# Kernel tuning notes

Measured on AMD Instinct MI355X. Metric: run time of the kernel, lower is better.

The kernel has to match this reference:

```python
import jax, jax.numpy as jnp
import numpy as np

N, E, F_IN, C, H12, H3, NCLS = 10000, 160000, 50, 256, 4, 6, 121


def gat_conv(x, src, dst, W, a_src, a_dst, b, heads, out_ch, concat, n):
    # x: [n, f_in]; W: [f_in, heads*out_ch]; a_*: [heads, out_ch]; src/dst: [e]
    h = (x @ W).reshape(n, heads, out_ch)
    # per-edge attention logits, LeakyReLU(0.2) as in PyG GATConv
    alpha = jax.nn.leaky_relu((h * a_src).sum(-1)[src] + (h * a_dst).sum(-1)[dst], 0.2)  # [e, heads]
    # segment softmax over incoming edges of each destination node
    amax = jax.ops.segment_max(alpha, dst, num_segments=n)
    ex = jnp.exp(alpha - amax[dst])
    denom = jax.ops.segment_sum(ex, dst, num_segments=n)
    w = ex / (denom[dst] + 1e-16)
    out = jax.ops.segment_sum(h[src] * w[..., None], dst, num_segments=n)  # [n, heads, out_ch]
    out = out.reshape(n, heads * out_ch) if concat else out.mean(axis=1)
    return out + b


def setup_inputs() -> dict:
    key = jax.random.key(0)
    ks = jax.random.split(key, 22)
    s = 0.05
    nrm = lambda k, shp: jax.random.normal(k, shp, jnp.float32) * s
    D = C * H12  # 1024
    return {
        "x": jax.random.normal(ks[0], (N, F_IN), jnp.float32),
        "edge_index": jax.random.randint(ks[1], (2, E), 0, N, dtype=jnp.int32),
        "W1": nrm(ks[2], (F_IN, H12 * C)), "a_src1": nrm(ks[3], (H12, C)), "a_dst1": nrm(ks[4], (H12, C)), "b1": jnp.zeros((H12 * C,), jnp.float32),
        "lW1": nrm(ks[5], (F_IN, D)), "lb1": jnp.zeros((D,), jnp.float32),
        "W2": nrm(ks[6], (D, H12 * C)), "a_src2": nrm(ks[7], (H12, C)), "a_dst2": nrm(ks[8], (H12, C)), "b2": jnp.zeros((H12 * C,), jnp.float32),
        "lW2": nrm(ks[9], (D, D)), "lb2": jnp.zeros((D,), jnp.float32),
        "W3": nrm(ks[10], (D, H3 * NCLS)), "a_src3": nrm(ks[11], (H3, NCLS)), "a_dst3": nrm(ks[12], (H3, NCLS)), "b3": jnp.zeros((NCLS,), jnp.float32),
        "lW3": nrm(ks[13], (D, NCLS)), "lb3": jnp.zeros((NCLS,), jnp.float32),
    }


def reference(x, edge_index, W1, a_src1, a_dst1, b1, lW1, lb1,
              W2, a_src2, a_dst2, b2, lW2, lb2,
              W3, a_src3, a_dst3, b3, lW3, lb3):
    n = x.shape[0]
    loop = jnp.arange(n, dtype=edge_index.dtype)  # self loops (PyG default)
    src = jnp.concatenate([edge_index[0], loop])
    dst = jnp.concatenate([edge_index[1], loop])
    h = jax.nn.elu(gat_conv(x, src, dst, W1, a_src1, a_dst1, b1, H12, C, True, n) + x @ lW1 + lb1)
    h = jax.nn.elu(gat_conv(h, src, dst, W2, a_src2, a_dst2, b2, H12, C, True, n) + h @ lW2 + lb2)
    return gat_conv(h, src, dst, W3, a_src3, a_dst3, b3, H3, NCLS, False, n) + h @ lW3 + lb3
```

## Files before the change

### kernel.cpp

```cpp
#include <hip/hip_runtime.h>
#include <cstdint>
#include <cstddef>

#define NN 10000
#define EE 160000
#define EN_ (EE + NN)
#define MPAD 10112
#define MT 79
#define CAP 512

typedef short s16x8 __attribute__((ext_vector_type(8)));
typedef float f32x4 __attribute__((ext_vector_type(4)));
typedef unsigned short u16;

__device__ __forceinline__ u16 f2bf(float f) {
  uint32_t u = __float_as_uint(f);
  uint32_t r = (u + 0x7fffu + ((u >> 16) & 1u)) >> 16;
  return (u16)r;
}
__device__ __forceinline__ float b2f(u16 u) {
  return __uint_as_float(((uint32_t)u) << 16);
}
__device__ __forceinline__ float b2f_lo(uint32_t p) { return __uint_as_float(p << 16); }
__device__ __forceinline__ float b2f_hi(uint32_t p) { return __uint_as_float(p & 0xffff0000u); }
__device__ __forceinline__ float lrelu02(float x) { return x > 0.f ? x : 0.2f * x; }
__device__ __forceinline__ float eluf(float x) { return x > 0.f ? x : (__expf(x) - 1.f); }

__global__ void k_count(const int* __restrict__ ei, int* __restrict__ cnt) {
  int e = blockIdx.x * blockDim.x + threadIdx.x;
  if (e >= EN_) return;
  int d = (e < EE) ? ei[EE + e] : (e - EE);
  atomicAdd(&cnt[d], 1);
}

__global__ __launch_bounds__(1024) void k_scan(const int* __restrict__ cnt, int* __restrict__ off) {
  __shared__ int sums[1024];
  int t = threadIdx.x;
  const int per = (NN + 1023) / 1024;
  int base = t * per;
  int local = 0;
  for (int j = 0; j < per; ++j) {
    int idx = base + j;
    if (idx < NN) local += cnt[idx];
  }
  sums[t] = local;
  __syncthreads();
  for (int s = 1; s < 1024; s <<= 1) {
    int v = (t >= s) ? sums[t - s] : 0;
    __syncthreads();
    sums[t] += v;
    __syncthreads();
  }
  int run = (t == 0) ? 0 : sums[t - 1];
  for (int j = 0; j < per; ++j) {
    int idx = base + j;
    if (idx < NN) { off[idx] = run; run += cnt[idx]; }
  }
  if (t == 1023) off[NN] = EN_;
}

__global__ void k_fill(const int* __restrict__ ei, const int* __restrict__ off,
                       int* __restrict__ cursor, int* __restrict__ csr_src) {
  int e = blockIdx.x * blockDim.x + threadIdx.x;
  if (e >= EN_) return;
  int s, d;
  if (e < EE) { s = ei[e]; d = ei[EE + e]; } else { s = d = e - EE; }
  int p = atomicAdd(&cursor[d], 1);
  csr_src[off[d] + p] = s;
}

#define PREP_BLOCKS 3490
__global__ __launch_bounds__(256) void k_prep(
    const float* __restrict__ x, u16* __restrict__ xb,
    const float* __restrict__ W1, const float* __restrict__ lW1,
    const float* __restrict__ W2, const float* __restrict__ lW2,
    const float* __restrict__ W3, const float* __restrict__ lW3,
    u16* __restrict__ wtc1, u16* __restrict__ wtc2, u16* __restrict__ wtc3,
    const float* __restrict__ lb1, const float* __restrict__ lb2,
    const float* __restrict__ lb3, float* __restrict__ fb,
    u16* __restrict__ bufX, int* __restrict__ cnt) {
  int b = blockIdx.x, t = threadIdx.x;
  if (b < 768) {
    const float* W; u16* Bt; int K, N, Kpad, nb, kb;
    if (b < 16)       { W = W1;  Bt = wtc1;                       K = 50;   N = 1024; Kpad = 64;   nb = b;      kb = 0; }
    else if (b < 32)  { W = lW1; Bt = wtc1 + (size_t)1024 * 64;   K = 50;   N = 1024; Kpad = 64;   nb = b - 16; kb = 0; }
    else if (b < 288) { int r = b - 32;  W = W2;  Bt = wtc2;                         K = 1024; N = 1024; Kpad = 1024; nb = r & 15; kb = r >> 4; }
    else if (b < 544) { int r = b - 288; W = lW2; Bt = wtc2 + (size_t)1024 * 1024;   K = 1024; N = 1024; Kpad = 1024; nb = r & 15; kb = r >> 4; }
    else if (b < 736) { int r = b - 544; W = W3;  Bt = wtc3;                         K = 1024; N = 726;  Kpad = 1024; nb = r % 12; kb = r / 12; }
    else              { int r = b - 736; W = lW3; Bt = wtc3 + (size_t)768 * 1024;    K = 1024; N = 121;  Kpad = 1024; nb = r & 1;  kb = r >> 1; }
    __shared__ float tile[64][65];
    int kbase = kb * 64, nbase = nb * 64;
    int nl = t & 63, kl0 = t >> 6;
#pragma unroll
    for (int j = 0; j < 16; ++j) {
      int k = kbase + kl0 + j * 4, n = nbase + nl;
      tile[kl0 + j * 4][nl] = (k < K && n < N) ? W[(size_t)k * N + n] : 0.f;
    }
    __syncthreads();
    int nr = t >> 2, kc = (t & 3) * 16;
    uint32_t pk[8];
#pragma unroll
    for (int j = 0; j < 8; ++j) {
      pk[j] = (uint32_t)f2bf(tile[kc + 2 * j][nr]) | ((uint32_t)f2bf(tile[kc + 2 * j + 1][nr]) << 16);
    }
    uint4* dst = (uint4*)(Bt + (size_t)(nbase + nr) * Kpad + kbase + kc);
    dst[0] = make_uint4(pk[0], pk[1], pk[2], pk[3]);
    dst[1] = make_uint4(pk[4], pk[5], pk[6], pk[7]);
  } else if (b < 3296) {
    int idx = (b - 768) * 256 + t;
    if (idx < MPAD * 64) {
      int m = idx >> 6, k = idx & 63;
      xb[idx] = f2bf((m < NN && k < 50) ? x[m * 50 + k] : 0.f);
    }
  } else if (b < 3352) {
    int idx = (b - 3296) * 256 + t;
    ((uint4*)(bufX + (size_t)NN * 1024))[idx] = make_uint4(0, 0, 0, 0);
  } else if (b < 3470) {
    int idx = (b - 3352) * 256 + t;
    if (idx < 3 * NN + 1) cnt[idx] = 0;
  } else {
    int idx = (b - 3470) * 256 + t;
    if (idx < 4992) {
      float v = 0.f;
      if (idx < 2048)      { if (idx >= 1024) v = lb1[idx - 1024]; }
      else if (idx < 4096) { int j = idx - 2048; if (j >= 1024) v = lb2[j - 1024]; }
      else                 { int j = idx - 4096; if (j >= 768 && j < 889) v = lb3[j - 768]; }
      fb[idx] = v;
    }
  }
}

template <int OUT_S_BF16>
__global__ __launch_bounds__(256) void k_gemm_fused(
    const u16* __restrict__ A, const u16* __restrict__ Bt,
    const float* __restrict__ fbias,
    u16* __restrict__ outH, int ldH,
    void* __restrict__ outS, int ldS, int nsplit, int nrealS,
    int M, int Kpad, int NS) {
  __shared__ __align__(16) u16 lA[128 * 64];
  __shared__ __align__(16) u16 lB[128 * 64];
  int bid = blockIdx.x;
  int xcd = bid & 7, seq = bid >> 3;
  int nIdx = seq % NS, mloc = seq / NS;
  int mIdx = mloc * 8 + xcd;
  if (mIdx >= MT) return;
  int bm = mIdx * 128, bn = nIdx * 128;

  int t = threadIdx.x;
  int wave = t >> 6, lane = t & 63;
  int wm = (wave >> 1) * 64, wn = (wave & 1) * 64;

  f32x4 acc[4][4];
#pragma unroll
  for (int i = 0; i < 4; ++i)
#pragma unroll
    for (int j = 0; j < 4; ++j)
#pragma unroll
      for (int r = 0; r < 4; ++r) acc[i][j][r] = 0.f;

  int row = lane & 15, quad = lane >> 4;

  for (int k0 = 0; k0 < Kpad; k0 += 64) {
#pragma unroll
    for (int is = 0; is < 4; ++is) {
      int L = is * 256 + t;
      int m = L >> 3, c = L & 7;
      int j = c ^ (m & 7);
      const u16* gpA = A + (size_t)(bm + m) * Kpad + k0 + j * 8;
      const u16* gpB = Bt + (size_t)(bn + m) * Kpad + k0 + j * 8;
      u16* lpA = lA + (size_t)(is * 256 + wave * 64) * 8;
      u16* lpB = lB + (size_t)(is * 256 + wave * 64) * 8;
      __builtin_amdgcn_global_load_lds(
          (const __attribute__((address_space(1))) void*)gpA,
          (__attribute__((address_space(3))) void*)lpA, 16, 0, 0);
      __builtin_amdgcn_global_load_lds(
          (const __attribute__((address_space(1))) void*)gpB,
          (__attribute__((address_space(3))) void*)lpB, 16, 0, 0);
    }
    __syncthreads();

#pragma unroll
    for (int kk = 0; kk < 2; ++kk) {
      s16x8 af[4], bf[4];
#pragma unroll
      for (int mi = 0; mi < 4; ++mi) {
        int m = wm + mi * 16 + row;
        int c = (kk * 4 + quad) ^ (m & 7);
        af[mi] = *(const s16x8*)&lA[m * 64 + c * 8];
      }
#pragma unroll
      for (int ni = 0; ni < 4; ++ni) {
        int n = wn + ni * 16 + row;
        int c = (kk * 4 + quad) ^ (n & 7);
        bf[ni] = *(const s16x8*)&lB[n * 64 + c * 8];
      }
#pragma unroll
      for (int mi = 0; mi < 4; ++mi)
#pragma unroll
        for (int ni = 0; ni < 4; ++ni)
          acc[mi][ni] = __builtin_amdgcn_mfma_f32_16x16x32_bf16(af[mi], bf[ni], acc[mi][ni], 0, 0, 0);
    }
    __syncthreads();
  }

  int col = lane & 15, qr = (lane >> 4) * 4;
  bool isH = bn < nsplit;
#pragma unroll
  for (int mi = 0; mi < 4; ++mi) {
#pragma unroll
    for (int r = 0; r < 4; ++r) {
      int m = bm + wm + mi * 16 + qr + r;
      if (m >= M) continue;
#pragma unroll
      for (int ni = 0; ni < 4; ++ni) {
        int n = bn + wn + ni * 16 + col;
        float v = acc[mi][ni][r] + fbias[n];
        if (isH) {
          outH[(size_t)m * ldH + n] = f2bf(v);
        } else {
          int c = n - nsplit;
          if (c < nrealS) {
            if (OUT_S_BF16) ((u16*)outS)[(size_t)m * ldS + c] = f2bf(v);
            else ((float*)outS)[(size_t)m * ldS + c] = v;
          }
        }
      }
    }
  }
}

__global__ void k_scores256(const u16* __restrict__ h, const float* __restrict__ a_src,
                            const float* __restrict__ a_dst, float* __restrict__ as_,
                            float* __restrict__ ad_) {
  int wid = (blockIdx.x * blockDim.x + threadIdx.x) >> 6;
  int lane = threadIdx.x & 63;
  if (wid >= NN * 4) return;
  int i = wid >> 2, hh = wid & 3;
  uint2 pk = *(const uint2*)(h + (size_t)i * 1024 + hh * 256 + 4 * lane);
  float4 av = *(const float4*)(a_src + hh * 256 + 4 * lane);
  float4 dv = *(const float4*)(a_dst + hh * 256 + 4 * lane);
  float x0 = b2f_lo(pk.x), x1 = b2f_hi(pk.x), x2 = b2f_lo(pk.y), x3 = b2f_hi(pk.y);
  float s1 = x0 * av.x + x1 * av.y + x2 * av.z + x3 * av.w;
  float s2 = x0 * dv.x + x1 * dv.y + x2 * dv.z + x3 * dv.w;
#pragma unroll
  for (int o = 32; o; o >>= 1) {
    s1 += __shfl_down(s1, o);
    s2 += __shfl_down(s2, o);
  }
  if (lane == 0) { as_[wid] = s1; ad_[wid] = s2; }
}

__global__ void k_scores(const u16* __restrict__ h, const float* __restrict__ a_src,
                         const float* __restrict__ a_dst, float* __restrict__ as_,
                         float* __restrict__ ad_, int H, int C, int ld) {
  int wid = (blockIdx.x * blockDim.x + threadIdx.x) >> 6;
  int lane = threadIdx.x & 63;
  if (wid >= NN * H) return;
  int i = wid / H, hh = wid - i * H;
  const u16* hp = h + (size_t)i * ld + hh * C;
  const float* sp = a_src + hh * C;
  const float* dp = a_dst + hh * C;
  float s1 = 0.f, s2 = 0.f;
  for (int c = lane; c < C; c += 64) {
    float v = b2f(hp[c]);
    s1 += v * sp[c];
    s2 += v * dp[c];
  }
#pragma unroll
  for (int o = 32; o; o >>= 1) {
    s1 += __shfl_down(s1, o);
    s2 += __shfl_down(s2, o);
  }
  if (lane == 0) { as_[wid] = s1; ad_[wid] = s2; }
}

__global__ __launch_bounds__(256) void k_agg_cat(
    const u16* __restrict__ h, const float* __restrict__ as_, const float* __restrict__ ad_,
    const int* __restrict__ off, const int* __restrict__ csr_src,
    const float* __restrict__ bias, const u16* __restrict__ skip, u16* __restrict__ outx) {
  const int F = 1024;
  int i = blockIdx.x, t = threadIdx.x;
  int start = off[i], end = off[i + 1];
  int wave = t >> 6, lane = t & 63;
  __shared__ int src_s[CAP];
  __shared__ float a_s[CAP][4];
  __shared__ float nm_s[4];
  float4 adv = *(const float4*)(ad_ + (size_t)i * 4);
  int hj = wave;
  float m_old = -1e30f;
  float denom = 0.f;
  float acc0 = 0.f, acc1 = 0.f, acc2 = 0.f, acc3 = 0.f;
  for (int e0 = start; e0 < end; e0 += CAP) {
    int ne = min(CAP, end - e0);
    __syncthreads();
    for (int j = t; j < ne; j += 256) {
      int s = csr_src[e0 + j];
      src_s[j] = s;
      float4 av = *(const float4*)(as_ + (size_t)s * 4);
      a_s[j][0] = lrelu02(av.x + adv.x);
      a_s[j][1] = lrelu02(av.y + adv.y);
      a_s[j][2] = lrelu02(av.z + adv.z);
      a_s[j][3] = lrelu02(av.w + adv.w);
    }
    __syncthreads();
    float cm = -1e30f;
    for (int j = lane; j < ne; j += 64) cm = fmaxf(cm, a_s[j][hj]);
#pragma unroll
    for (int o = 32; o; o >>= 1) cm = fmaxf(cm, __shfl_down(cm, o));
    if (lane == 0) nm_s[hj] = fmaxf(m_old, cm);
    __syncthreads();
    float nm0 = nm_s[0], nm1 = nm_s[1], nm2 = nm_s[2], nm3 = nm_s[3];
    for (int j = t; j < ne; j += 256) {
      a_s[j][0] = __expf(a_s[j][0] - nm0);
      a_s[j][1] = __expf(a_s[j][1] - nm1);
      a_s[j][2] = __expf(a_s[j][2] - nm2);
      a_s[j][3] = __expf(a_s[j][3] - nm3);
    }
    __syncthreads();
    float cd = 0.f;
    for (int j = lane; j < ne; j += 64) cd += a_s[j][hj];
#pragma unroll
    for (int o = 32; o; o >>= 1) cd += __shfl_down(cd, o);
    cd = __shfl(cd, 0);
    float nm = nm_s[hj];
    float rs = __expf(m_old - nm);
    acc0 *= rs; acc1 *= rs; acc2 *= rs; acc3 *= rs;
    denom = denom * rs + cd;
    m_old = nm;
#pragma unroll 4
    for (int e = 0; e < ne; ++e) {
      const u16* hp = h + (size_t)src_s[e] * F;
      uint2 pk = *(const uint2*)(hp + 4 * t);
      float ww = a_s[e][hj];
      acc0 += ww * b2f_lo(pk.x);
      acc1 += ww * b2f_hi(pk.x);
      acc2 += ww * b2f_lo(pk.y);
      acc3 += ww * b2f_hi(pk.y);
    }
  }
  float rdm = 1.f / (denom + 1e-16f);
  int ch = 4 * t;
  float4 bb = *(const float4*)(bias + ch);
  uint2 sk = *(const uint2*)(skip + (size_t)i * F + ch);
  u16 o0 = f2bf(eluf(acc0 * rdm + bb.x + b2f_lo(sk.x)));
  u16 o1 = f2bf(eluf(acc1 * rdm + bb.y + b2f_hi(sk.x)));
  u16 o2 = f2bf(eluf(acc2 * rdm + bb.z + b2f_lo(sk.y)));
  u16 o3 = f2bf(eluf(acc3 * rdm + bb.w + b2f_hi(sk.y)));
  uint2 ov;
  ov.x = (uint32_t)o0 | ((uint32_t)o1 << 16);
  ov.y = (uint32_t)o2 | ((uint32_t)o3 << 16);
  *(uint2*)(outx + (size_t)i * F + ch) = ov;
}

__global__ __launch_bounds__(256) void k_agg_mean(
    const u16* __restrict__ h, const float* __restrict__ as_, const float* __restrict__ ad_,
    const int* __restrict__ off, const int* __restrict__ csr_src,
    const float* __restrict__ bias, float* __restrict__ out) {
  const int H = 6, C = 121, FP = 768;
  int i = blockIdx.x, t = threadIdx.x;
  int start = off[i], end = off[i + 1];
  int wave = t >> 6, lane = t & 63;
  __shared__ int src_s[CAP];
  __shared__ float a_s[CAP][H];
  __shared__ float nm_s[H], mo_s[H], d_s[H];
  __shared__ float agg_s[FP];
  float adv[H];
  {
    float2 v0 = *(const float2*)(ad_ + (size_t)i * H);
    float2 v1 = *(const float2*)(ad_ + (size_t)i * H + 2);
    float2 v2 = *(const float2*)(ad_ + (size_t)i * H + 4);
    adv[0] = v0.x; adv[1] = v0.y; adv[2] = v1.x; adv[3] = v1.y; adv[4] = v2.x; adv[5] = v2.y;
  }
  if (t < H) { mo_s[t] = -1e30f; d_s[t] = 0.f; }
  int c0 = 4 * t;
  bool act = t < 192;
  int hd[4];
#pragma unroll
  for (int r = 0; r < 4; ++r) {
    int c = c0 + r;
    hd[r] = (act && c < 726) ? (c / C) : 0;
  }
  float acc[4] = {0.f, 0.f, 0.f, 0.f};
  for (int e0 = start; e0 < end; e0 += CAP) {
    int ne = min(CAP, end - e0);
    __syncthreads();
    for (int j = t; j < ne; j += 256) {
      int s = csr_src[e0 + j];
      src_s[j] = s;
      float2 v0 = *(const float2*)(as_ + (size_t)s * H);
      float2 v1 = *(const float2*)(as_ + (size_t)s * H + 2);
      float2 v2 = *(const float2*)(as_ + (size_t)s * H + 4);
      a_s[j][0] = lrelu02(v0.x + adv[0]);
      a_s[j][1] = lrelu02(v0.y + adv[1]);
      a_s[j][2] = lrelu02(v1.x + adv[2]);
      a_s[j][3] = lrelu02(v1.y + adv[3]);
      a_s[j][4] = lrelu02(v2.x + adv[4]);
      a_s[j][5] = lrelu02(v2.y + adv[5]);
    }
    __syncthreads();
    for (int hh = wave; hh < H; hh += 4) {
      float cm = -1e30f;
      for (int j = lane; j < ne; j += 64) cm = fmaxf(cm, a_s[j][hh]);
#pragma unroll
      for (int o = 32; o; o >>= 1) cm = fmaxf(cm, __shfl_down(cm, o));
      if (lane == 0) nm_s[hh] = fmaxf(mo_s[hh], cm);
    }
    __syncthreads();
#pragma unroll
    for (int r = 0; r < 4; ++r) acc[r] *= __expf(mo_s[hd[r]] - nm_s[hd[r]]);
    for (int j = t; j < ne; j += 256) {
#pragma unroll
      for (int hh = 0; hh < H; ++hh) a_s[j][hh] = __expf(a_s[j][hh] - nm_s[hh]);
    }
    __syncthreads();
    for (int hh = wave; hh < H; hh += 4) {
      float cd = 0.f;
      for (int j = lane; j < ne; j += 64) cd += a_s[j][hh];
#pragma unroll
      for (int o = 32; o; o >>= 1) cd += __shfl_down(cd, o);
      if (lane == 0) {
        d_s[hh] = d_s[hh] * __expf(mo_s[hh] - nm_s[hh]) + cd;
        mo_s[hh] = nm_s[hh];
      }
    }
    if (act) {
#pragma unroll 4
      for (int e = 0; e < ne; ++e) {
        const u16* hp = h + (size_t)src_s[e] * FP;
        uint2 pk = *(const uint2*)(hp + c0);
        acc[0] += a_s[e][hd[0]] * b2f_lo(pk.x);
        acc[1] += a_s[e][hd[1]] * b2f_hi(pk.x);
        acc[2] += a_s[e][hd[2]] * b2f_lo(pk.y);
        acc[3] += a_s[e][hd[3]] * b2f_hi(pk.y);
      }
    }
  }
  __syncthreads();
  if (act) {
#pragma unroll
    for (int r = 0; r < 4; ++r) agg_s[c0 + r] = acc[r] / (d_s[hd[r]] + 1e-16f);
  }
  __syncthreads();
  if (t < C) {
    float s = 0.f;
#pragma unroll
    for (int hh = 0; hh < H; ++hh) s += agg_s[hh * C + t];
    size_t idx = (size_t)i * C + t;
    out[idx] += s * (1.f / 6.f) + bias[t];
  }
}

extern "C" void kernel_launch(void* const* d_in, const int* in_sizes, int n_in,
                              void* d_out, int out_size, void* d_ws, size_t ws_size,
                              hipStream_t stream) {
  const float* x = (const float*)d_in[0];
  const int* ei = (const int*)d_in[1];
  const float* W1 = (const float*)d_in[2];
  const float* a_src1 = (const float*)d_in[3];
  const float* a_dst1 = (const float*)d_in[4];
  const float* b1 = (const float*)d_in[5];
  const float* lW1 = (const float*)d_in[6];
  const float* lb1 = (const float*)d_in[7];
  const float* W2 = (const float*)d_in[8];
  const float* a_src2 = (const float*)d_in[9];
  const float* a_dst2 = (const float*)d_in[10];
  const float* b2 = (const float*)d_in[11];
  const float* lW2 = (const float*)d_in[12];
  const float* lb2 = (const float*)d_in[13];
  const float* W3 = (const float*)d_in[14];
  const float* a_src3 = (const float*)d_in[15];
  const float* a_dst3 = (const float*)d_in[16];
  const float* b3 = (const float*)d_in[17];
  const float* lW3 = (const float*)d_in[18];
  const float* lb3 = (const float*)d_in[19];
  float* outp = (float*)d_out;

  char* ws = (char*)d_ws;
  size_t o = 0;
  auto alloc = [&](size_t bytes) { void* p = ws + o; o += (bytes + 255) & ~(size_t)255; return p; };
  u16* bufH = (u16*)alloc((size_t)MPAD * 1024 * 2);
  u16* bufX = (u16*)alloc((size_t)MPAD * 1024 * 2);
  u16* bufS = (u16*)alloc((size_t)NN * 1024 * 2);
  u16* xb16 = (u16*)alloc((size_t)MPAD * 64 * 2);
  u16* wtc1 = (u16*)alloc((size_t)2048 * 64 * 2);
  u16* wtc2 = (u16*)alloc((size_t)2048 * 1024 * 2);
  u16* wtc3 = (u16*)alloc((size_t)896 * 1024 * 2);
  float* fb12 = (float*)alloc((size_t)4992 * 4);
  float* fb1 = fb12;
  float* fb2 = fb12 + 2048;
  float* fb3 = fb12 + 4096;
  float* as_ = (float*)alloc((size_t)NN * 6 * 4);
  float* ad_ = (float*)alloc((size_t)NN * 6 * 4);
  int* cnt = (int*)alloc((size_t)(3 * NN + 1) * 4);
  int* offs = cnt + NN;
  int* cursor = offs + NN + 1;
  int* csr_src = (int*)alloc((size_t)EN_ * 4);

  k_prep<<<PREP_BLOCKS, 256, 0, stream>>>(x, xb16, W1, lW1, W2, lW2, W3, lW3,
                                          wtc1, wtc2, wtc3, lb1, lb2, lb3, fb12,
                                          bufX, cnt);
  int eb = (EN_ + 255) / 256;
  k_count<<<eb, 256, 0, stream>>>(ei, cnt);
  k_scan<<<1, 1024, 0, stream>>>(cnt, offs);
  k_fill<<<eb, 256, 0, stream>>>(ei, offs, cursor, csr_src);

  {
    k_gemm_fused<1><<<16 * 80, 256, 0, stream>>>(
        xb16, wtc1, fb1, bufH, 1024, bufS, 1024, 1024, 1024, NN, 64, 16);
    k_scores256<<<10000, 256, 0, stream>>>(bufH, a_src1, a_dst1, as_, ad_);
    k_agg_cat<<<NN, 256, 0, stream>>>(bufH, as_, ad_, offs, csr_src, b1, bufS, bufX);
  }
  {
    k_gemm_fused<1><<<16 * 80, 256, 0, stream>>>(
        bufX, wtc2, fb2, bufH, 1024, bufS, 1024, 1024, 1024, NN, 1024, 16);
    k_scores256<<<10000, 256, 0, stream>>>(bufH, a_src2, a_dst2, as_, ad_);
    k_agg_cat<<<NN, 256, 0, stream>>>(bufH, as_, ad_, offs, csr_src, b2, bufS, bufX);
  }
  {
    k_gemm_fused<0><<<7 * 80, 256, 0, stream>>>(
        bufX, wtc3, fb3, bufH, 768, outp, 121, 768, 121, NN, 1024, 7);
    k_scores<<<(NN * 6 + 3) / 4, 256, 0, stream>>>(bufH, a_src3, a_dst3, as_, ad_, 6, 121, 768);
    k_agg_mean<<<NN, 256, 0, stream>>>(bufH, as_, ad_, offs, csr_src, b3, outp);
  }
}
```

Measured before the change: 445.8 us.

## Store projected node features in FP8 to halve gather traffic

The GEMM epilogue now writes the projected features h as FP8 (e4m3, clamped to ±448) instead of bf16. The score and aggregation kernels load 4 bytes per thread and convert with the hardware fp8-to-f32 instruction. This halves the bytes moved in the edge gather, the dominant memory traffic, and shrinks the per-block shared edge buffer from 512 to 128 entries. The cost is a large precision loss on h, which may push results past the tolerance, and degree chunks that overflow the smaller buffer take extra rescale passes.

```diff
diff --git a/kernel.cpp b/kernel.cpp
--- a/kernel.cpp
+++ b/kernel.cpp
@@ -7,11 +7,12 @@
 #define EN_ (EE + NN)
 #define MPAD 10112
 #define MT 79
-#define CAP 512
+#define CAP 128
 
 typedef short s16x8 __attribute__((ext_vector_type(8)));
 typedef float f32x4 __attribute__((ext_vector_type(4)));
 typedef unsigned short u16;
+typedef unsigned char u8;
 
 __device__ __forceinline__ u16 f2bf(float f) {
   uint32_t u = __float_as_uint(f);
@@ -25,6 +26,10 @@
 __device__ __forceinline__ float b2f_hi(uint32_t p) { return __uint_as_float(p & 0xffff0000u); }
 __device__ __forceinline__ float lrelu02(float x) { return x > 0.f ? x : 0.2f * x; }
 __device__ __forceinline__ float eluf(float x) { return x > 0.f ? x : (__expf(x) - 1.f); }
+__device__ __forceinline__ u8 f2fp8(float v) {
+  v = fminf(fmaxf(v, -448.f), 448.f);
+  return (u8)(__builtin_amdgcn_cvt_pk_fp8_f32(v, v, 0, false) & 0xff);
+}
 
 __global__ void k_count(const int* __restrict__ ei, int* __restrict__ cnt) {
   int e = blockIdx.x * blockDim.x + threadIdx.x;
@@ -134,7 +139,7 @@
 __global__ __launch_bounds__(256) void k_gemm_fused(
     const u16* __restrict__ A, const u16* __restrict__ Bt,
     const float* __restrict__ fbias,
-    u16* __restrict__ outH, int ldH,
+    u8* __restrict__ outH, int ldH,
     void* __restrict__ outS, int ldS, int nsplit, int nrealS,
     int M, int Kpad, int NS) {
   __shared__ __align__(16) u16 lA[128 * 64];
@@ -216,7 +221,7 @@
         int n = bn + wn + ni * 16 + col;
         float v = acc[mi][ni][r] + fbias[n];
         if (isH) {
-          outH[(size_t)m * ldH + n] = f2bf(v);
+          outH[(size_t)m * ldH + n] = f2fp8(v);
         } else {
           int c = n - nsplit;
           if (c < nrealS) {
@@ -229,17 +234,20 @@
   }
 }
 
-__global__ void k_scores256(const u16* __restrict__ h, const float* __restrict__ a_src,
+__global__ void k_scores256(const u8* __restrict__ h, const float* __restrict__ a_src,
                             const float* __restrict__ a_dst, float* __restrict__ as_,
                             float* __restrict__ ad_) {
   int wid = (blockIdx.x * blockDim.x + threadIdx.x) >> 6;
   int lane = threadIdx.x & 63;
   if (wid >= NN * 4) return;
   int i = wid >> 2, hh = wid & 3;
-  uint2 pk = *(const uint2*)(h + (size_t)i * 1024 + hh * 256 + 4 * lane);
+  int pk = *(const int*)(h + (size_t)i * 1024 + hh * 256 + 4 * lane);
   float4 av = *(const float4*)(a_src + hh * 256 + 4 * lane);
   float4 dv = *(const float4*)(a_dst + hh * 256 + 4 * lane);
-  float x0 = b2f_lo(pk.x), x1 = b2f_hi(pk.x), x2 = b2f_lo(pk.y), x3 = b2f_hi(pk.y);
+  float x0 = __builtin_amdgcn_cvt_f32_fp8(pk, 0);
+  float x1 = __builtin_amdgcn_cvt_f32_fp8(pk, 1);
+  float x2 = __builtin_amdgcn_cvt_f32_fp8(pk, 2);
+  float x3 = __builtin_amdgcn_cvt_f32_fp8(pk, 3);
   float s1 = x0 * av.x + x1 * av.y + x2 * av.z + x3 * av.w;
   float s2 = x0 * dv.x + x1 * dv.y + x2 * dv.z + x3 * dv.w;
 #pragma unroll
@@ -250,19 +258,19 @@
   if (lane == 0) { as_[wid] = s1; ad_[wid] = s2; }
 }
 
-__global__ void k_scores(const u16* __restrict__ h, const float* __restrict__ a_src,
+__global__ void k_scores(const u8* __restrict__ h, const float* __restrict__ a_src,
                          const float* __restrict__ a_dst, float* __restrict__ as_,
                          float* __restrict__ ad_, int H, int C, int ld) {
   int wid = (blockIdx.x * blockDim.x + threadIdx.x) >> 6;
   int lane = threadIdx.x & 63;
   if (wid >= NN * H) return;
   int i = wid / H, hh = wid - i * H;
-  const u16* hp = h + (size_t)i * ld + hh * C;
+  const u8* hp = h + (size_t)i * ld + hh * C;
   const float* sp = a_src + hh * C;
   const float* dp = a_dst + hh * C;
   float s1 = 0.f, s2 = 0.f;
   for (int c = lane; c < C; c += 64) {
-    float v = b2f(hp[c]);
+    float v = __builtin_amdgcn_cvt_f32_fp8((int)hp[c], 0);
     s1 += v * sp[c];
     s2 += v * dp[c];
   }
@@ -275,7 +283,7 @@
 }
 
 __global__ __launch_bounds__(256) void k_agg_cat(
-    const u16* __restrict__ h, const float* __restrict__ as_, const float* __restrict__ ad_,
+    const u8* __restrict__ h, const float* __restrict__ as_, const float* __restrict__ ad_,
     const int* __restrict__ off, const int* __restrict__ csr_src,
     const float* __restrict__ bias, const u16* __restrict__ skip, u16* __restrict__ outx) {
   const int F = 1024;
@@ -329,13 +337,13 @@
     m_old = nm;
 #pragma unroll 4
     for (int e = 0; e < ne; ++e) {
-      const u16* hp = h + (size_t)src_s[e] * F;
-      uint2 pk = *(const uint2*)(hp + 4 * t);
+      const u8* hp = h + (size_t)src_s[e] * F;
+      int pk = *(const int*)(hp + 4 * t);
       float ww = a_s[e][hj];
-      acc0 += ww * b2f_lo(pk.x);
-      acc1 += ww * b2f_hi(pk.x);
-      acc2 += ww * b2f_lo(pk.y);
-      acc3 += ww * b2f_hi(pk.y);
+      acc0 += ww * __builtin_amdgcn_cvt_f32_fp8(pk, 0);
+      acc1 += ww * __builtin_amdgcn_cvt_f32_fp8(pk, 1);
+      acc2 += ww * __builtin_amdgcn_cvt_f32_fp8(pk, 2);
+      acc3 += ww * __builtin_amdgcn_cvt_f32_fp8(pk, 3);
     }
   }
   float rdm = 1.f / (denom + 1e-16f);
@@ -353,7 +361,7 @@
 }
 
 __global__ __launch_bounds__(256) void k_agg_mean(
-    const u16* __restrict__ h, const float* __restrict__ as_, const float* __restrict__ ad_,
+    const u8* __restrict__ h, const float* __restrict__ as_, const float* __restrict__ ad_,
     const int* __restrict__ off, const int* __restrict__ csr_src,
     const float* __restrict__ bias, float* __restrict__ out) {
   const int H = 6, C = 121, FP = 768;
@@ -426,12 +434,12 @@
     if (act) {
 #pragma unroll 4
       for (int e = 0; e < ne; ++e) {
-        const u16* hp = h + (size_t)src_s[e] * FP;
-        uint2 pk = *(const uint2*)(hp + c0);
-        acc[0] += a_s[e][hd[0]] * b2f_lo(pk.x);
-        acc[1] += a_s[e][hd[1]] * b2f_hi(pk.x);
-        acc[2] += a_s[e][hd[2]] * b2f_lo(pk.y);
-        acc[3] += a_s[e][hd[3]] * b2f_hi(pk.y);
+        const u8* hp = h + (size_t)src_s[e] * FP;
+        int pk = *(const int*)(hp + c0);
+        acc[0] += a_s[e][hd[0]] * __builtin_amdgcn_cvt_f32_fp8(pk, 0);
+        acc[1] += a_s[e][hd[1]] * __builtin_amdgcn_cvt_f32_fp8(pk, 1);
+        acc[2] += a_s[e][hd[2]] * __builtin_amdgcn_cvt_f32_fp8(pk, 2);
+        acc[3] += a_s[e][hd[3]] * __builtin_amdgcn_cvt_f32_fp8(pk, 3);
       }
     }
   }
@@ -478,7 +486,7 @@
   char* ws = (char*)d_ws;
   size_t o = 0;
   auto alloc = [&](size_t bytes) { void* p = ws + o; o += (bytes + 255) & ~(size_t)255; return p; };
-  u16* bufH = (u16*)alloc((size_t)MPAD * 1024 * 2);
+  u8* bufH8 = (u8*)alloc((size_t)MPAD * 1024);
   u16* bufX = (u16*)alloc((size_t)MPAD * 1024 * 2);
   u16* bufS = (u16*)alloc((size_t)NN * 1024 * 2);
   u16* xb16 = (u16*)alloc((size_t)MPAD * 64 * 2);
@@ -506,20 +514,20 @@
 
   {
     k_gemm_fused<1><<<16 * 80, 256, 0, stream>>>(
-        xb16, wtc1, fb1, bufH, 1024, bufS, 1024, 1024, 1024, NN, 64, 16);
-    k_scores256<<<10000, 256, 0, stream>>>(bufH, a_src1, a_dst1, as_, ad_);
-    k_agg_cat<<<NN, 256, 0, stream>>>(bufH, as_, ad_, offs, csr_src, b1, bufS, bufX);
+        xb16, wtc1, fb1, bufH8, 1024, bufS, 1024, 1024, 1024, NN, 64, 16);
+    k_scores256<<<10000, 256, 0, stream>>>(bufH8, a_src1, a_dst1, as_, ad_);
+    k_agg_cat<<<NN, 256, 0, stream>>>(bufH8, as_, ad_, offs, csr_src, b1, bufS, bufX);
   }
   {
     k_gemm_fused<1><<<16 * 80, 256, 0, stream>>>(
-        bufX, wtc2, fb2, bufH, 1024, bufS, 1024, 1024, 1024, NN, 1024, 16);
-    k_scores256<<<10000, 256, 0, stream>>>(bufH, a_src2, a_dst2, as_, ad_);
-    k_agg_cat<<<NN, 256, 0, stream>>>(bufH, as_, ad_, offs, csr_src, b2, bufS, bufX);
+        bufX, wtc2, fb2, bufH8, 1024, bufS, 1024, 1024, 1024, NN, 1024, 16);
+    k_scores256<<<10000, 256, 0, stream>>>(bufH8, a_src2, a_dst2, as_, ad_);
+    k_agg_cat<<<NN, 256, 0, stream>>>(bufH8, as_, ad_, offs, csr_src, b2, bufS, bufX);
   }
   {
     k_gemm_fused<0><<<7 * 80, 256, 0, stream>>>(
-        bufX, wtc3, fb3, bufH, 768, outp, 121, 768, 121, NN, 1024, 7);
-    k_scores<<<(NN * 6 + 3) / 4, 256, 0, stream>>>(bufH, a_src3, a_dst3, as_, ad_, 6, 121, 768);
-    k_agg_mean<<<NN, 256, 0, stream>>>(bufH, as_, ad_, offs, csr_src, b3, outp);
-  }
-}
+        bufX, wtc3, fb3, bufH8, 768, outp, 121, 768, 121, NN, 1024, 7);
+    k_scores<<<(NN * 6 + 3) / 4, 256, 0, stream>>>(bufH8, a_src3, a_dst3, as_, ad_, 6, 121, 768);
+    k_agg_mean<<<NN, 256, 0, stream>>>(bufH8, as_, ad_, offs, csr_src, b3, outp);
+  }
+}
```

Result: faster. 402.0 us (-9.8%).
